# Kernel tuning notes

Hardware: AMD Instinct MI355X
Metric: run time of the kernel (lower is better)

The kernel has to match this reference:

```python
import jax, jax.numpy as jnp
import numpy as np

B, T, N, F, H = 2048, 50, 23, 4, 64
FUTURE = 10


def setup_inputs() -> dict:
    key = jax.random.key(0)
    ks = jax.random.split(key, 12)
    return {
        "x_seq": jax.random.normal(ks[0], (B, T, N, F), jnp.float32),
        "adj_seq": jax.random.uniform(ks[1], (B, T, N, N), jnp.float32),
        "W_gcn": jax.random.normal(ks[2], (H, F), jnp.float32) * 0.1,
        "b_gcn": jax.random.normal(ks[3], (H,), jnp.float32) * 0.1,
        "W_ih": jax.random.normal(ks[4], (3 * H, H), jnp.float32) * 0.1,
        "W_hh": jax.random.normal(ks[5], (3 * H, H), jnp.float32) * 0.1,
        "b_ih": jax.random.normal(ks[6], (3 * H,), jnp.float32) * 0.1,
        "b_hh": jax.random.normal(ks[7], (3 * H,), jnp.float32) * 0.1,
        "W_d1": jax.random.normal(ks[8], (H // 2, H), jnp.float32) * 0.1,
        "b_d1": jax.random.normal(ks[9], (H // 2,), jnp.float32) * 0.1,
        "W_d2": jax.random.normal(ks[10], (F, H // 2), jnp.float32) * 0.1,
        "b_d2": jax.random.normal(ks[11], (F,), jnp.float32) * 0.1,
        "future_steps": FUTURE,
    }


def reference(x_seq, adj_seq, W_gcn, b_gcn, W_ih, W_hh, b_ih, b_hh,
              W_d1, b_d1, W_d2, b_d2, future_steps):
    def gru_cell(x, h):
        # torch.nn.GRUCell gate order: r, z, n
        gi = x @ W_ih.T + b_ih          # [B,N,3H]
        gh = h @ W_hh.T + b_hh
        i_r, i_z, i_n = jnp.split(gi, 3, axis=-1)
        h_r, h_z, h_n = jnp.split(gh, 3, axis=-1)
        r = jax.nn.sigmoid(i_r + h_r)
        z = jax.nn.sigmoid(i_z + h_z)
        n = jnp.tanh(i_n + r * h_n)
        return (1.0 - z) * n + z * h

    def st_cell(x, adj, h):
        support = x @ W_gcn.T + b_gcn               # [B,N,H]
        spatial = jax.nn.relu(adj @ support)        # bmm aggregation + relu
        return gru_cell(spatial, h)

    def decode(h):
        return jax.nn.relu(h @ W_d1.T + b_d1) @ W_d2.T + b_d2

    # encode history
    h0 = jnp.zeros((x_seq.shape[0], x_seq.shape[2], W_gcn.shape[0]), x_seq.dtype)
    xs = jnp.moveaxis(x_seq, 1, 0)      # [T,B,N,F]
    adjs = jnp.moveaxis(adj_seq, 1, 0)  # [T,B,N,N]

    def hist_step(h, inp):
        xt, at = inp
        return st_cell(xt, at, h), None

    h_t, _ = jax.lax.scan(hist_step, h0, (xs, adjs))

    adj_last = adj_seq[:, -1]
    x_last = x_seq[:, -1]

    def fut_step(carry, _):
        h, x = carry
        h = st_cell(x, adj_last, h)
        nx = decode(h)
        return (h, nx), nx

    _, preds = jax.lax.scan(fut_step, (h_t, x_last), None, length=future_steps)
    return jnp.moveaxis(preds, 0, 1)    # [B, future_steps, N, F]
```

## Files before the change

### kernel.cpp

```cpp
#include <hip/hip_runtime.h>
#include <stdint.h>


typedef _Float16 f16;
typedef f16   f16x2  __attribute__((ext_vector_type(2)));
typedef f16   f16x8  __attribute__((ext_vector_type(8)));
typedef float f32x4n __attribute__((ext_vector_type(4)));
typedef float f32x16 __attribute__((ext_vector_type(16)));

#define WBYTES 69632
#define PW 4736
#define SMEM_BYTES (WBYTES + 8 * PW)

static __device__ __forceinline__ unsigned pk2(float a, float b) {
    f16x2 h; h[0] = (f16)a; h[1] = (f16)b;
    return __builtin_bit_cast(unsigned, h);
}
static __device__ __forceinline__ f16x8 mkfrag(unsigned a, unsigned b, unsigned c, unsigned d) {
    uint4 u = make_uint4(a, b, c, d);
    return __builtin_bit_cast(f16x8, u);
}
static __device__ __forceinline__ unsigned shx32(unsigned v) {
    return (unsigned)__shfl_xor((int)v, 32, 64);
}
static __device__ __forceinline__ float sigm(float x) {
    return __builtin_amdgcn_rcpf(1.f + __expf(-x));
}
static __device__ __forceinline__ float tanhp(float x) {
    return 1.f - 2.f * __builtin_amdgcn_rcpf(1.f + __expf(2.f * x));
}
static __device__ __forceinline__ void cvt_tile(const f32x16& v, int hf, f16x8& fe, f16x8& fo) {
    unsigned u0 = pk2(v[0], v[1]),  u1 = pk2(v[2], v[3]);
    unsigned u2 = pk2(v[4], v[5]),  u3 = pk2(v[6], v[7]);
    unsigned u4 = pk2(v[8], v[9]),  u5 = pk2(v[10], v[11]);
    unsigned u6 = pk2(v[12], v[13]), u7 = pk2(v[14], v[15]);
    unsigned sA = shx32(hf ? u0 : u2), sB = shx32(hf ? u1 : u3);
    unsigned sC = shx32(hf ? u4 : u6), sD = shx32(hf ? u5 : u7);
    fe = mkfrag(hf ? sA : u0, hf ? sB : u1, hf ? u2 : sA, hf ? u3 : sB);
    fo = mkfrag(hf ? sC : u4, hf ? sD : u5, hf ? u6 : sC, hf ? u7 : sD);
}

__global__ __launch_bounds__(512, 2) void gwm_kernel(
    const float* __restrict__ xseq, const float* __restrict__ adjseq,
    const float* __restrict__ Wg,  const float* __restrict__ bg,
    const float* __restrict__ Wih, const float* __restrict__ Whh,
    const float* __restrict__ bih, const float* __restrict__ bhh,
    const float* __restrict__ Wd1, const float* __restrict__ bd1,
    const float* __restrict__ Wd2, const float* __restrict__ bd2,
    float* __restrict__ out)
{
    extern __shared__ char smem[];
    const int tid  = threadIdx.x;
    const int lane = tid & 63;
    const int wv   = tid >> 6;
    const int l31  = lane & 31;
    const int hf   = lane >> 5;

    for (int idx = tid; idx < 68 * 64; idx += 512) {
        const int fi = idx >> 6, l = idx & 63, ln = l & 31, lh = l >> 5;
        float v[8];
        #pragma unroll
        for (int j = 0; j < 8; ++j) v[j] = 0.f;
        if (fi < 60) {
            const int grp = fi / 5, kt = fi - grp * 5;
            const int side = grp / 6, tau = grp - side * 6;
            const float* W = side ? Whh : Wih;
            const int row = tau * 32 + ln;
            if (kt < 4) {
                const float* s = W + row * 64 + kt * 16 + lh * 8;
                #pragma unroll
                for (int j = 0; j < 8; ++j) v[j] = s[j];
            } else if (lh == 0) {
                if (side == 0) v[0] = bih[row] + (tau < 4 ? bhh[row] : 0.f);
                else           v[0] = (tau < 4) ? 0.f : bhh[row];
            }
        } else if (fi < 65) {
            const int kt = fi - 60;
            if (kt < 4) {
                const float* s = Wd1 + ln * 64 + kt * 16 + lh * 8;
                #pragma unroll
                for (int j = 0; j < 8; ++j) v[j] = s[j];
            } else if (lh == 0) v[0] = bd1[ln];
        } else {
            const int kt = fi - 65;
            if (kt < 2) {
                if (ln < 4) {
                    const float* s = Wd2 + ln * 32 + kt * 16 + lh * 8;
                    #pragma unroll
                    for (int j = 0; j < 8; ++j) v[j] = s[j];
                }
            } else if (lh == 0 && ln < 4) v[0] = bd2[ln];
        }
        f16x8 h8;
        #pragma unroll
        for (int j = 0; j < 8; ++j) h8[j] = (f16)v[j];
        *(f16x8*)(smem + fi * 1024 + l * 16) = h8;
    }

    char*  wbase = smem + WBYTES + wv * PW;
    float* xL    = (float*)wbase;
    float* adjF  = (float*)(wbase + 512);

    {
        f32x4n z4; z4[0] = z4[1] = z4[2] = z4[3] = 0.f;
        #pragma unroll
        for (int q = 0; q < 4; ++q) *(f32x4n*)(adjF + lane * 16 + q * 4) = z4;
        adjF[1024 + lane] = 0.f;
        if (lane < 32) adjF[1024 + 64 + lane] = 0.f;
        if (lane < 64) { if (lane + 64 < 128) xL[lane + 64] = 0.f; xL[lane] = 0.f; }
    }
    __syncthreads();

    const f16x8 bC = (hf == 0) ? mkfrag(pk2(1.f, 0.f), 0u, 0u, 0u)
                               : mkfrag(0u, 0u, 0u, 0u);
    f16x8 aWg0, aWg1;
    {
        const int c0 = l31, c1 = 32 + l31;
        aWg0 = hf ? mkfrag(0u,0u,0u,0u)
                  : mkfrag(pk2(Wg[c0*4], Wg[c0*4+1]), pk2(Wg[c0*4+2], Wg[c0*4+3]),
                           pk2(bg[c0], 0.f), 0u);
        aWg1 = hf ? mkfrag(0u,0u,0u,0u)
                  : mkfrag(pk2(Wg[c1*4], Wg[c1*4+1]), pk2(Wg[c1*4+2], Wg[c1*4+3]),
                           pk2(bg[c1], 0.f), 0u);
    }

    const int b = blockIdx.x * 8 + wv;
    const float* xg = xseq   + (size_t)b * (50 * 92);
    const float* ag = adjseq + (size_t)b * (50 * 529);
    float* outb = out + (size_t)b * 920;

    float pf[9]; f32x4n pfx;
    #pragma unroll
    for (int r = 0; r < 9; ++r) pf[r] = 0.f;
    pfx[0] = pfx[1] = pfx[2] = pfx[3] = 0.f;
    #pragma unroll
    for (int r = 0; r < 9; ++r) if (r < 8 || lane < 17) pf[r] = ag[lane + 64 * r];
    if (lane < 23) pfx = *(const f32x4n*)(xg + 4 * lane);

    f32x16 hC0, hC1;
    f16x8  bH[4];
    #pragma unroll
    for (int i = 0; i < 16; ++i) { hC0[i] = 0.f; hC1[i] = 0.f; }
    #pragma unroll
    for (int kt = 0; kt < 4; ++kt) bH[kt] = mkfrag(0u, 0u, 0u, 0u);

    f32x16 z16;
    #pragma unroll
    for (int i = 0; i < 16; ++i) z16[i] = 0.f;

    auto mm = [&](f32x16 acc, int fi, f16x8 bfr) -> f32x16 {
        const f16x8 aW = *(const f16x8*)(smem + fi * 1024 + lane * 16);
        return __builtin_amdgcn_mfma_f32_32x32x16_f16(aW, bfr, acc, 0, 0, 0);
    };

    for (int t = 0; t < 60; ++t) {
        if (t < 50) {
            #pragma unroll
            for (int r = 0; r < 9; ++r) {
                if (r < 8 || lane < 17) {
                    const unsigned e = (unsigned)(lane + 64 * r);
                    const unsigned row = __umulhi(e, 186737709u);
                    const unsigned col = e - row * 23u;
                    adjF[row * 33 + col] = pf[r];
                }
            }
            if (lane < 23) *(f32x4n*)(xL + 4 * lane) = pfx;
            if (t + 1 < 50) {
                const float* a2 = ag + (t + 1) * 529;
                #pragma unroll
                for (int r = 0; r < 9; ++r) if (r < 8 || lane < 17) pf[r] = a2[lane + 64 * r];
                if (lane < 23) pfx = *(const f32x4n*)(xg + (t + 1) * 92 + 4 * lane);
            }
        }

        f16x8 aX0, aX1;
        {
            float v0[8], v1[8];
            #pragma unroll
            for (int j = 0; j < 8; ++j) {
                const int n0 = 8 * hf + j, n1 = 16 + 8 * hf + j;
                const float x0 = xL[n0 * 4 + (l31 & 3)];
                const float x1 = xL[n1 * 4 + (l31 & 3)];
                v0[j] = (l31 < 4) ? x0 : ((l31 == 4) ? 1.f : 0.f);
                v1[j] = (l31 < 4) ? x1 : ((l31 == 4) ? 1.f : 0.f);
            }
            aX0 = mkfrag(pk2(v0[0],v0[1]), pk2(v0[2],v0[3]), pk2(v0[4],v0[5]), pk2(v0[6],v0[7]));
            aX1 = mkfrag(pk2(v1[0],v1[1]), pk2(v1[2],v1[3]), pk2(v1[4],v1[5]), pk2(v1[6],v1[7]));
        }
        f16x8 bA0, bA1;
        {
            float a0[8], a1[8];
            #pragma unroll
            for (int j = 0; j < 8; ++j) {
                a0[j] = adjF[l31 * 33 + 8 * hf + j];
                a1[j] = adjF[l31 * 33 + 16 + 8 * hf + j];
            }
            bA0 = mkfrag(pk2(a0[0],a0[1]), pk2(a0[2],a0[3]), pk2(a0[4],a0[5]), pk2(a0[6],a0[7]));
            bA1 = mkfrag(pk2(a1[0],a1[1]), pk2(a1[2],a1[3]), pk2(a1[4],a1[5]), pk2(a1[6],a1[7]));
        }
        f32x16 accE = z16;
        accE = __builtin_amdgcn_mfma_f32_32x32x16_f16(aX0, bA0, accE, 0, 0, 0);
        accE = __builtin_amdgcn_mfma_f32_32x32x16_f16(aX1, bA1, accE, 0, 0, 0);
        const unsigned p01 = pk2(accE[0], accE[1]), p23 = pk2(accE[2], accE[3]);
        const unsigned p4  = shx32(hf ? pk2(accE[0], 0.f) : 0u);
        const f16x8 bE = hf ? mkfrag(0u, 0u, 0u, 0u) : mkfrag(p01, p23, p4, 0u);
        f32x16 s0 = z16, s1 = z16;
        s0 = __builtin_amdgcn_mfma_f32_32x32x16_f16(aWg0, bE, s0, 0, 0, 0);
        s1 = __builtin_amdgcn_mfma_f32_32x32x16_f16(aWg1, bE, s1, 0, 0, 0);
        #pragma unroll
        for (int i = 0; i < 16; ++i) { s0[i] = fmaxf(s0[i], 0.f); s1[i] = fmaxf(s1[i], 0.f); }
        f16x8 bS[4];
        cvt_tile(s0, hf, bS[0], bS[1]);
        cvt_tile(s1, hf, bS[2], bS[3]);

        f16x8 nb0, nb1, nb2, nb3;
        #pragma unroll
        for (int hnum = 0; hnum < 2; ++hnum) {
            const int tR = hnum, tZ = 2 + hnum, tN = 4 + hnum;
            f32x16 aR = z16, aZ = z16, aNi = z16, aNh = z16;
            #pragma unroll
            for (int kt = 0; kt < 4; ++kt) {
                aR  = mm(aR,  (0 * 6 + tR) * 5 + kt, bS[kt]);
                aR  = mm(aR,  (1 * 6 + tR) * 5 + kt, bH[kt]);
                aZ  = mm(aZ,  (0 * 6 + tZ) * 5 + kt, bS[kt]);
                aZ  = mm(aZ,  (1 * 6 + tZ) * 5 + kt, bH[kt]);
                aNi = mm(aNi, (0 * 6 + tN) * 5 + kt, bS[kt]);
                aNh = mm(aNh, (1 * 6 + tN) * 5 + kt, bH[kt]);
            }
            aR  = mm(aR,  (0 * 6 + tR) * 5 + 4, bC);
            aZ  = mm(aZ,  (0 * 6 + tZ) * 5 + 4, bC);
            aNi = mm(aNi, (0 * 6 + tN) * 5 + 4, bC);
            aNh = mm(aNh, (1 * 6 + tN) * 5 + 4, bC);
            f32x16& hv = hnum ? hC1 : hC0;
            #pragma unroll
            for (int i = 0; i < 16; ++i) {
                const float r = sigm(aR[i]);
                const float z = sigm(aZ[i]);
                const float n = tanhp(aNi[i] + r * aNh[i]);
                hv[i] = n + z * (hv[i] - n);
            }
            if (hnum == 0) cvt_tile(hC0, hf, nb0, nb1);
            else           cvt_tile(hC1, hf, nb2, nb3);
        }
        bH[0] = nb0; bH[1] = nb1; bH[2] = nb2; bH[3] = nb3;

        if (t >= 50) {
            const int fs = t - 50;
            f32x16 d1 = z16;
            #pragma unroll
            for (int kt = 0; kt < 4; ++kt) d1 = mm(d1, 60 + kt, bH[kt]);
            d1 = mm(d1, 64, bC);
            #pragma unroll
            for (int i = 0; i < 16; ++i) d1[i] = fmaxf(d1[i], 0.f);
            f16x8 bD0, bD1;
            cvt_tile(d1, hf, bD0, bD1);
            f32x16 d2 = z16;
            d2 = mm(d2, 65, bD0);
            d2 = mm(d2, 66, bD1);
            d2 = mm(d2, 67, bC);
            if (hf == 0 && l31 < 23) {
                f32x4n o;
                o[0] = d2[0]; o[1] = d2[1]; o[2] = d2[2]; o[3] = d2[3];
                *(f32x4n*)(outb + fs * 92 + l31 * 4) = o;
                *(f32x4n*)(xL + l31 * 4) = o;
            }
        }
    }
}

extern "C" void kernel_launch(void* const* d_in, const int* in_sizes, int n_in,
                              void* d_out, int out_size, void* d_ws, size_t ws_size,
                              hipStream_t stream) {
    (void)in_sizes; (void)n_in; (void)d_ws; (void)ws_size; (void)out_size;
    hipFuncSetAttribute((const void*)gwm_kernel,
                        hipFuncAttributeMaxDynamicSharedMemorySize, SMEM_BYTES);
    gwm_kernel<<<dim3(256), dim3(512), SMEM_BYTES, stream>>>(
        (const float*)d_in[0], (const float*)d_in[1], (const float*)d_in[2],
        (const float*)d_in[3], (const float*)d_in[4], (const float*)d_in[5],
        (const float*)d_in[6], (const float*)d_in[7], (const float*)d_in[8],
        (const float*)d_in[9], (const float*)d_in[10], (const float*)d_in[11],
        (float*)d_out);
}
```

Baseline: 558.4 us.

## Software-pipeline GRU steps, load adjacency straight into registers, use permlane32 swaps

Restructures the time loop so the spatial GCN path for step t+1 is computed between the two GRU half-tiles of step t, overlapping MFMA chains with activation math. Adjacency rows are now loaded directly from global into MFMA B-fragment registers, which removes the LDS staging buffer and cuts per-wave shared memory. Cross-half shuffles are replaced with permlane32_swap. This raises register pressure and leaves a separate tail step and rollout loop.

```diff
diff --git a/kernel.cpp b/kernel.cpp
--- a/kernel.cpp
+++ b/kernel.cpp
@@ -7,9 +7,11 @@
 typedef f16   f16x8  __attribute__((ext_vector_type(8)));
 typedef float f32x4n __attribute__((ext_vector_type(4)));
 typedef float f32x16 __attribute__((ext_vector_type(16)));
+typedef int   i32x2  __attribute__((ext_vector_type(2)));
+typedef float f32x4u __attribute__((ext_vector_type(4), aligned(4)));
 
 #define WBYTES 69632
-#define PW 4736
+#define PW 512
 #define SMEM_BYTES (WBYTES + 8 * PW)
 
 static __device__ __forceinline__ unsigned pk2(float a, float b) {
@@ -20,24 +22,30 @@
     uint4 u = make_uint4(a, b, c, d);
     return __builtin_bit_cast(f16x8, u);
 }
-static __device__ __forceinline__ unsigned shx32(unsigned v) {
-    return (unsigned)__shfl_xor((int)v, 32, 64);
-}
+static __device__ __forceinline__ void pswap2(unsigned a, unsigned b,
+                                              unsigned& r0, unsigned& r1) {
+    auto r = __builtin_amdgcn_permlane32_swap((int)a, (int)b, false, false);
+    i32x2 v = __builtin_bit_cast(i32x2, r);
+    r0 = (unsigned)v[0]; r1 = (unsigned)v[1];
+}
+static __device__ __forceinline__ unsigned dup_hi(unsigned x) {
+    unsigned r0, r1; pswap2(x, x, r0, r1); return r1;
+}
+
 static __device__ __forceinline__ float sigm(float x) {
     return __builtin_amdgcn_rcpf(1.f + __expf(-x));
 }
 static __device__ __forceinline__ float tanhp(float x) {
     return 1.f - 2.f * __builtin_amdgcn_rcpf(1.f + __expf(2.f * x));
 }
-static __device__ __forceinline__ void cvt_tile(const f32x16& v, int hf, f16x8& fe, f16x8& fo) {
-    unsigned u0 = pk2(v[0], v[1]),  u1 = pk2(v[2], v[3]);
-    unsigned u2 = pk2(v[4], v[5]),  u3 = pk2(v[6], v[7]);
-    unsigned u4 = pk2(v[8], v[9]),  u5 = pk2(v[10], v[11]);
-    unsigned u6 = pk2(v[12], v[13]), u7 = pk2(v[14], v[15]);
-    unsigned sA = shx32(hf ? u0 : u2), sB = shx32(hf ? u1 : u3);
-    unsigned sC = shx32(hf ? u4 : u6), sD = shx32(hf ? u5 : u7);
-    fe = mkfrag(hf ? sA : u0, hf ? sB : u1, hf ? u2 : sA, hf ? u3 : sB);
-    fo = mkfrag(hf ? sC : u4, hf ? sD : u5, hf ? u6 : sC, hf ? u7 : sD);
+static __device__ __forceinline__ void cvt_tile(const f32x16& v, f16x8& fe, f16x8& fo) {
+    unsigned e0, e1, e2, e3, o0, o1, o2, o3;
+    pswap2(pk2(v[0], v[1]),   pk2(v[4], v[5]),   e0, e2);
+    pswap2(pk2(v[2], v[3]),   pk2(v[6], v[7]),   e1, e3);
+    pswap2(pk2(v[8], v[9]),   pk2(v[12], v[13]), o0, o2);
+    pswap2(pk2(v[10], v[11]), pk2(v[14], v[15]), o1, o3);
+    fe = mkfrag(e0, e1, e2, e3);
+    fo = mkfrag(o0, o1, o2, o3);
 }
 
 __global__ __launch_bounds__(512, 2) void gwm_kernel(
@@ -97,18 +105,8 @@
         *(f16x8*)(smem + fi * 1024 + l * 16) = h8;
     }
 
-    char*  wbase = smem + WBYTES + wv * PW;
-    float* xL    = (float*)wbase;
-    float* adjF  = (float*)(wbase + 512);
-
-    {
-        f32x4n z4; z4[0] = z4[1] = z4[2] = z4[3] = 0.f;
-        #pragma unroll
-        for (int q = 0; q < 4; ++q) *(f32x4n*)(adjF + lane * 16 + q * 4) = z4;
-        adjF[1024 + lane] = 0.f;
-        if (lane < 32) adjF[1024 + 64 + lane] = 0.f;
-        if (lane < 64) { if (lane + 64 < 128) xL[lane + 64] = 0.f; xL[lane] = 0.f; }
-    }
+    float* xL = (float*)(smem + WBYTES + wv * PW);
+    xL[lane] = 0.f; xL[lane + 64] = 0.f;
     __syncthreads();
 
     const f16x8 bC = (hf == 0) ? mkfrag(pk2(1.f, 0.f), 0u, 0u, 0u)
@@ -129,16 +127,12 @@
     const float* ag = adjseq + (size_t)b * (50 * 529);
     float* outb = out + (size_t)b * 920;
 
-    float pf[9]; f32x4n pfx;
-    #pragma unroll
-    for (int r = 0; r < 9; ++r) pf[r] = 0.f;
-    pfx[0] = pfx[1] = pfx[2] = pfx[3] = 0.f;
-    #pragma unroll
-    for (int r = 0; r < 9; ++r) if (r < 8 || lane < 17) pf[r] = ag[lane + 64 * r];
-    if (lane < 23) pfx = *(const f32x4n*)(xg + 4 * lane);
-
     f32x16 hC0, hC1;
     f16x8  bH[4];
+    f16x8  bS[4];
+    f16x8  bA0, bA1;
+    float  c[16];
+    f32x4n pfx;
     #pragma unroll
     for (int i = 0; i < 16; ++i) { hC0[i] = 0.f; hC1[i] = 0.f; }
     #pragma unroll
@@ -153,26 +147,34 @@
         return __builtin_amdgcn_mfma_f32_32x32x16_f16(aW, bfr, acc, 0, 0, 0);
     };
 
-    for (int t = 0; t < 60; ++t) {
-        if (t < 50) {
-            #pragma unroll
-            for (int r = 0; r < 9; ++r) {
-                if (r < 8 || lane < 17) {
-                    const unsigned e = (unsigned)(lane + 64 * r);
-                    const unsigned row = __umulhi(e, 186737709u);
-                    const unsigned col = e - row * 23u;
-                    adjF[row * 33 + col] = pf[r];
-                }
+    auto load_adj = [&](int t) {
+        #pragma unroll
+        for (int i = 0; i < 16; ++i) c[i] = 0.f;
+        if (l31 < 23) {
+            const float* ar = ag + t * 529 + l31 * 23 + 8 * hf;
+            f32x4u u0 = *(const f32x4u*)ar;
+            f32x4u u1 = *(const f32x4u*)(ar + 4);
+            c[0]=u0[0]; c[1]=u0[1]; c[2]=u0[2]; c[3]=u0[3];
+            c[4]=u1[0]; c[5]=u1[1]; c[6]=u1[2]; c[7]=u1[3];
+            if (hf == 0) {
+                f32x4u u2 = *(const f32x4u*)(ar + 16);
+                c[8]=u2[0]; c[9]=u2[1]; c[10]=u2[2]; c[11]=u2[3];
+                c[12]=ar[20]; c[13]=ar[21]; c[14]=ar[22];
             }
-            if (lane < 23) *(f32x4n*)(xL + 4 * lane) = pfx;
-            if (t + 1 < 50) {
-                const float* a2 = ag + (t + 1) * 529;
-                #pragma unroll
-                for (int r = 0; r < 9; ++r) if (r < 8 || lane < 17) pf[r] = a2[lane + 64 * r];
-                if (lane < 23) pfx = *(const f32x4n*)(xg + (t + 1) * 92 + 4 * lane);
-            }
-        }
-
+        }
+    };
+    auto pack_adj = [&]() {
+        bA0 = mkfrag(pk2(c[0],c[1]),  pk2(c[2],c[3]),   pk2(c[4],c[5]),   pk2(c[6],c[7]));
+        bA1 = mkfrag(pk2(c[8],c[9]),  pk2(c[10],c[11]), pk2(c[12],c[13]), pk2(c[14],c[15]));
+    };
+    auto load_x  = [&](int t) {
+        if (lane < 23) pfx = *(const f32x4n*)(xg + t * 92 + 4 * lane);
+    };
+    auto stage_x = [&]() {
+        if (lane < 23) *(f32x4n*)(xL + 4 * lane) = pfx;
+    };
+
+    auto spath = [&](f16x8* bSo) {
         f16x8 aX0, aX1;
         {
             float v0[8], v1[8];
@@ -187,83 +189,109 @@
             aX0 = mkfrag(pk2(v0[0],v0[1]), pk2(v0[2],v0[3]), pk2(v0[4],v0[5]), pk2(v0[6],v0[7]));
             aX1 = mkfrag(pk2(v1[0],v1[1]), pk2(v1[2],v1[3]), pk2(v1[4],v1[5]), pk2(v1[6],v1[7]));
         }
-        f16x8 bA0, bA1;
-        {
-            float a0[8], a1[8];
-            #pragma unroll
-            for (int j = 0; j < 8; ++j) {
-                a0[j] = adjF[l31 * 33 + 8 * hf + j];
-                a1[j] = adjF[l31 * 33 + 16 + 8 * hf + j];
-            }
-            bA0 = mkfrag(pk2(a0[0],a0[1]), pk2(a0[2],a0[3]), pk2(a0[4],a0[5]), pk2(a0[6],a0[7]));
-            bA1 = mkfrag(pk2(a1[0],a1[1]), pk2(a1[2],a1[3]), pk2(a1[4],a1[5]), pk2(a1[6],a1[7]));
-        }
         f32x16 accE = z16;
         accE = __builtin_amdgcn_mfma_f32_32x32x16_f16(aX0, bA0, accE, 0, 0, 0);
         accE = __builtin_amdgcn_mfma_f32_32x32x16_f16(aX1, bA1, accE, 0, 0, 0);
         const unsigned p01 = pk2(accE[0], accE[1]), p23 = pk2(accE[2], accE[3]);
-        const unsigned p4  = shx32(hf ? pk2(accE[0], 0.f) : 0u);
+        const unsigned p4  = dup_hi(pk2(accE[0], 0.f));
         const f16x8 bE = hf ? mkfrag(0u, 0u, 0u, 0u) : mkfrag(p01, p23, p4, 0u);
         f32x16 s0 = z16, s1 = z16;
         s0 = __builtin_amdgcn_mfma_f32_32x32x16_f16(aWg0, bE, s0, 0, 0, 0);
         s1 = __builtin_amdgcn_mfma_f32_32x32x16_f16(aWg1, bE, s1, 0, 0, 0);
         #pragma unroll
         for (int i = 0; i < 16; ++i) { s0[i] = fmaxf(s0[i], 0.f); s1[i] = fmaxf(s1[i], 0.f); }
-        f16x8 bS[4];
-        cvt_tile(s0, hf, bS[0], bS[1]);
-        cvt_tile(s1, hf, bS[2], bS[3]);
-
+        cvt_tile(s0, bSo[0], bSo[1]);
+        cvt_tile(s1, bSo[2], bSo[3]);
+    };
+
+    auto gru_mfma = [&](int hnum, f32x16& aR, f32x16& aZ, f32x16& aNi, f32x16& aNh) {
+        const int tR = hnum, tZ = 2 + hnum, tN = 4 + hnum;
+        aR = z16; aZ = z16; aNi = z16; aNh = z16;
+        #pragma unroll
+        for (int kt = 0; kt < 4; ++kt) {
+            aR  = mm(aR,  (0 * 6 + tR) * 5 + kt, bS[kt]);
+            aR  = mm(aR,  (1 * 6 + tR) * 5 + kt, bH[kt]);
+            aZ  = mm(aZ,  (0 * 6 + tZ) * 5 + kt, bS[kt]);
+            aZ  = mm(aZ,  (1 * 6 + tZ) * 5 + kt, bH[kt]);
+            aNi = mm(aNi, (0 * 6 + tN) * 5 + kt, bS[kt]);
+            aNh = mm(aNh, (1 * 6 + tN) * 5 + kt, bH[kt]);
+        }
+        aR  = mm(aR,  (0 * 6 + tR) * 5 + 4, bC);
+        aZ  = mm(aZ,  (0 * 6 + tZ) * 5 + 4, bC);
+        aNi = mm(aNi, (0 * 6 + tN) * 5 + 4, bC);
+        aNh = mm(aNh, (1 * 6 + tN) * 5 + 4, bC);
+    };
+    auto act = [&](f32x16& hv, const f32x16& aR, const f32x16& aZ,
+                   const f32x16& aNi, const f32x16& aNh, f16x8& nbe, f16x8& nbo) {
+        #pragma unroll
+        for (int i = 0; i < 16; ++i) {
+            const float r = sigm(aR[i]);
+            const float z = sigm(aZ[i]);
+            const float n = tanhp(aNi[i] + r * aNh[i]);
+            hv[i] = n + z * (hv[i] - n);
+        }
+        cvt_tile(hv, nbe, nbo);
+    };
+
+    load_x(0); stage_x();
+    load_adj(0); pack_adj();
+    load_x(1);
+    spath(bS);
+    load_adj(1);
+
+    for (int t = 0; t < 49; ++t) {
+        f32x16 aR0, aZ0, aNi0, aNh0, aR1, aZ1, aNi1, aNh1;
+        f16x8 nb0, nb1, nb2, nb3, nS[4];
+        gru_mfma(0, aR0, aZ0, aNi0, aNh0);
+        stage_x();
+        act(hC0, aR0, aZ0, aNi0, aNh0, nb0, nb1);
+        pack_adj();
+        const int tp = (t + 2 < 50) ? t + 2 : 49;
+        load_adj(tp); load_x(tp);
+        spath(nS);
+        gru_mfma(1, aR1, aZ1, aNi1, aNh1);
+        act(hC1, aR1, aZ1, aNi1, aNh1, nb2, nb3);
+        bH[0] = nb0; bH[1] = nb1; bH[2] = nb2; bH[3] = nb3;
+        bS[0] = nS[0]; bS[1] = nS[1]; bS[2] = nS[2]; bS[3] = nS[3];
+    }
+
+    {
+        f32x16 aR0, aZ0, aNi0, aNh0, aR1, aZ1, aNi1, aNh1;
         f16x8 nb0, nb1, nb2, nb3;
-        #pragma unroll
-        for (int hnum = 0; hnum < 2; ++hnum) {
-            const int tR = hnum, tZ = 2 + hnum, tN = 4 + hnum;
-            f32x16 aR = z16, aZ = z16, aNi = z16, aNh = z16;
-            #pragma unroll
-            for (int kt = 0; kt < 4; ++kt) {
-                aR  = mm(aR,  (0 * 6 + tR) * 5 + kt, bS[kt]);
-                aR  = mm(aR,  (1 * 6 + tR) * 5 + kt, bH[kt]);
-                aZ  = mm(aZ,  (0 * 6 + tZ) * 5 + kt, bS[kt]);
-                aZ  = mm(aZ,  (1 * 6 + tZ) * 5 + kt, bH[kt]);
-                aNi = mm(aNi, (0 * 6 + tN) * 5 + kt, bS[kt]);
-                aNh = mm(aNh, (1 * 6 + tN) * 5 + kt, bH[kt]);
-            }
-            aR  = mm(aR,  (0 * 6 + tR) * 5 + 4, bC);
-            aZ  = mm(aZ,  (0 * 6 + tZ) * 5 + 4, bC);
-            aNi = mm(aNi, (0 * 6 + tN) * 5 + 4, bC);
-            aNh = mm(aNh, (1 * 6 + tN) * 5 + 4, bC);
-            f32x16& hv = hnum ? hC1 : hC0;
-            #pragma unroll
-            for (int i = 0; i < 16; ++i) {
-                const float r = sigm(aR[i]);
-                const float z = sigm(aZ[i]);
-                const float n = tanhp(aNi[i] + r * aNh[i]);
-                hv[i] = n + z * (hv[i] - n);
-            }
-            if (hnum == 0) cvt_tile(hC0, hf, nb0, nb1);
-            else           cvt_tile(hC1, hf, nb2, nb3);
-        }
+        gru_mfma(0, aR0, aZ0, aNi0, aNh0);
+        act(hC0, aR0, aZ0, aNi0, aNh0, nb0, nb1);
+        gru_mfma(1, aR1, aZ1, aNi1, aNh1);
+        act(hC1, aR1, aZ1, aNi1, aNh1, nb2, nb3);
         bH[0] = nb0; bH[1] = nb1; bH[2] = nb2; bH[3] = nb3;
-
-        if (t >= 50) {
-            const int fs = t - 50;
-            f32x16 d1 = z16;
-            #pragma unroll
-            for (int kt = 0; kt < 4; ++kt) d1 = mm(d1, 60 + kt, bH[kt]);
-            d1 = mm(d1, 64, bC);
-            #pragma unroll
-            for (int i = 0; i < 16; ++i) d1[i] = fmaxf(d1[i], 0.f);
-            f16x8 bD0, bD1;
-            cvt_tile(d1, hf, bD0, bD1);
-            f32x16 d2 = z16;
-            d2 = mm(d2, 65, bD0);
-            d2 = mm(d2, 66, bD1);
-            d2 = mm(d2, 67, bC);
-            if (hf == 0 && l31 < 23) {
-                f32x4n o;
-                o[0] = d2[0]; o[1] = d2[1]; o[2] = d2[2]; o[3] = d2[3];
-                *(f32x4n*)(outb + fs * 92 + l31 * 4) = o;
-                *(f32x4n*)(xL + l31 * 4) = o;
-            }
+    }
+
+    for (int fs = 0; fs < 10; ++fs) {
+        spath(bS);
+        f32x16 aR0, aZ0, aNi0, aNh0, aR1, aZ1, aNi1, aNh1;
+        f16x8 nb0, nb1, nb2, nb3;
+        gru_mfma(0, aR0, aZ0, aNi0, aNh0);
+        act(hC0, aR0, aZ0, aNi0, aNh0, nb0, nb1);
+        gru_mfma(1, aR1, aZ1, aNi1, aNh1);
+        act(hC1, aR1, aZ1, aNi1, aNh1, nb2, nb3);
+        bH[0] = nb0; bH[1] = nb1; bH[2] = nb2; bH[3] = nb3;
+
+        f32x16 d1 = z16;
+        #pragma unroll
+        for (int kt = 0; kt < 4; ++kt) d1 = mm(d1, 60 + kt, bH[kt]);
+        d1 = mm(d1, 64, bC);
+        #pragma unroll
+        for (int i = 0; i < 16; ++i) d1[i] = fmaxf(d1[i], 0.f);
+        f16x8 bD0, bD1;
+        cvt_tile(d1, bD0, bD1);
+        f32x16 d2 = z16;
+        d2 = mm(d2, 65, bD0);
+        d2 = mm(d2, 66, bD1);
+        d2 = mm(d2, 67, bC);
+        if (hf == 0 && l31 < 23) {
+            f32x4n o;
+            o[0] = d2[0]; o[1] = d2[1]; o[2] = d2[2]; o[3] = d2[3];
+            *(f32x4n*)(outb + fs * 92 + l31 * 4) = o;
+            *(f32x4n*)(xL + l31 * 4) = o;
         }
     }
 }
```

Measured after the change: 733.7 us. 1.31x slower.
